# Kernel optimization log

Hardware: AMD Instinct MI355X
Metric: run time of the kernel (lower is better)

The kernel has to match this reference:

```python
import jax, jax.numpy as jnp
import numpy as np

B, NB, H, E, NCT, NL = 16, 4096, 128, 65536, 32, 2
LN_EPS = 1e-5


def _layernorm(x, scale, bias):
    mu = jnp.mean(x, axis=-1, keepdims=True)
    var = jnp.var(x, axis=-1, keepdims=True)
    return (x - mu) / jnp.sqrt(var + LN_EPS) * scale + bias


def setup_inputs() -> dict:
    key = jax.random.key(0)
    ks = jax.random.split(key, 18)
    s = 1.0 / np.sqrt(H)
    inp = {
        'block_tokens': jax.random.normal(ks[0], (B, NB, H), jnp.float32),
        'edge_structure': jnp.full((E,), 0.5, jnp.float32),
        'ct_emb': 0.1 * jax.random.normal(ks[1], (NCT, E), jnp.float32),
        'W_proj': s * jax.random.normal(ks[2], (H, H), jnp.float32),
        'b_proj': jnp.zeros((H,), jnp.float32),
        'W_gate': (1.0 / np.sqrt(2 * H)) * jax.random.normal(ks[3], (2 * H, H), jnp.float32),
        'b_gate': jnp.zeros((H,), jnp.float32),
        'ln_scale': jnp.ones((NL, H), jnp.float32),
        'ln_bias': jnp.zeros((NL, H), jnp.float32),
        'W1': s * jax.random.normal(ks[4], (NL, H, 2 * H), jnp.float32),
        'b1': jnp.zeros((NL, 2 * H), jnp.float32),
        'W2': (1.0 / np.sqrt(2 * H)) * jax.random.normal(ks[5], (NL, 2 * H, H), jnp.float32),
        'b2': jnp.zeros((NL, H), jnp.float32),
        'cancer_type': jax.random.randint(ks[6], (B,), 0, NCT),
        'edge_src': jax.random.randint(ks[7], (E,), 0, NB),
        'edge_dst': jax.random.randint(ks[8], (E,), 0, NB),
        'block_active': jax.random.bernoulli(ks[9], 0.9, (B, NB)),
    }
    return inp


def reference(block_tokens, edge_structure, ct_emb, W_proj, b_proj, W_gate, b_gate,
              ln_scale, ln_bias, W1, b1, W2, b2,
              cancer_type, edge_src, edge_dst, block_active):
    # per-edge signed weights, masked by active src/dst blocks  -> (B, E)
    structure = jax.nn.sigmoid(edge_structure)
    edge_w = structure[None, :] * ct_emb[cancer_type]
    edge_w = edge_w * block_active[:, edge_src].astype(edge_w.dtype) \
                    * block_active[:, edge_dst].astype(edge_w.dtype)
    # route projection + ELU
    h_route = jax.nn.elu(jnp.einsum('bnh,hd->bnd', block_tokens, W_proj) + b_proj)
    # gather sources, weight, scatter-add to destinations
    weighted = edge_w[..., None] * h_route[:, edge_src, :]          # (B, E, H)
    messages = jnp.zeros_like(block_tokens).at[:, edge_dst, :].add(weighted)
    # gated residual
    gate = jax.nn.sigmoid(
        jnp.einsum('bnh,hd->bnd', jnp.concatenate([block_tokens, messages], axis=-1), W_gate) + b_gate)
    x = block_tokens + gate * messages
    # norm + FFN layers (dropout is identity at inference)
    for l in range(NL):
        normed = _layernorm(x, ln_scale[l], ln_bias[l])
        h = jax.nn.elu(jnp.einsum('bnh,hf->bnf', normed, W1[l]) + b1[l])
        x = x + jnp.einsum('bnf,fh->bnh', h, W2[l]) + b2[l]
    return (x, edge_w)
```

## Files before the change

kernel.cpp:

```cpp
#include <hip/hip_runtime.h>
#include <hip/hip_bf16.h>

#define BB     16
#define NBLK   4096
#define HD     128
#define NE     65536
#define MTOT   (BB * NBLK)

typedef __attribute__((ext_vector_type(8))) short bf16x8;
typedef __attribute__((ext_vector_type(4))) float f32x4;

__device__ __forceinline__ float bf2f(unsigned short u) {
    union { unsigned int i; float f; } v; v.i = ((unsigned int)u) << 16; return v.f;
}
__device__ __forceinline__ unsigned short f2bf(float f) {
    union { float f; unsigned int i; } v; v.f = f;
    unsigned int u = v.i;
    unsigned int r = u + 0x7FFFu + ((u >> 16) & 1u);
    return (unsigned short)(r >> 16);
}
__device__ __forceinline__ float ldf(const void* p, size_t i, int f32m) {
    return f32m ? ((const float*)p)[i] : bf2f(((const unsigned short*)p)[i]);
}
__device__ __forceinline__ int get_active(const void* p, int i, int mode) {
    switch (mode) {
        case 1:  return ((const unsigned char*)p)[i] != 0;
        case 2:  return ((const unsigned short*)p)[i] != 0;
        case 3:  return ((const float*)p)[i] != 0.f;
        default: return ((const int*)p)[i] != 0;
    }
}

__global__ void probe_k(const unsigned int* __restrict__ es,
                        const unsigned int* __restrict__ act,
                        int* __restrict__ flags)
{
    const int lane = threadIdx.x;
    const unsigned int v0 = act[lane], v1 = act[64 + lane];
    auto le1  = [](unsigned int v) { return v <= 1u; };
    auto byt  = [](unsigned int v) {
        return ((v & 0xFFu) <= 1u) && (((v >> 8) & 0xFFu) <= 1u) &&
               (((v >> 16) & 0xFFu) <= 1u) && ((v >> 24) <= 1u); };
    auto f32b = [](unsigned int v) { return v == 0u || v == 0x3F800000u; };
    auto bfb  = [](unsigned int v) {
        unsigned short h0 = (unsigned short)(v & 0xFFFFu), h1 = (unsigned short)(v >> 16);
        return (h0 == 0u || h0 == 0x3F80u) && (h1 == 0u || h1 == 0x3F80u); };
    const unsigned long long m_le1 = __ballot(le1(v0) && le1(v1));
    const unsigned long long m_byt = __ballot(byt(v0) && byt(v1));
    const unsigned long long m_f32 = __ballot(f32b(v0) && f32b(v1));
    const unsigned long long m_bf  = __ballot(bfb(v0) && bfb(v1));
    if (lane == 0) {
        flags[0] = (es[0] != 0x3F003F00u) ? 1 : 0;
        const unsigned long long full = ~0ull;
        flags[1] = (m_le1 == full) ? 0
                 : (m_byt == full) ? 1
                 : (m_f32 == full) ? 3
                 : (m_bf  == full) ? 2 : 0;
    }
}

__global__ __launch_bounds__(256) void cvt_k(const void* __restrict__ bt,
                                             unsigned short* __restrict__ bt16,
                                             const int* __restrict__ flags)
{
    const size_t i = ((size_t)blockIdx.x * 256 + threadIdx.x) * 8;
    if (flags[0]) {
        const float* q = (const float*)bt + i;
        f32x4 lo = *(const f32x4*)q;
        f32x4 hi = *(const f32x4*)(q + 4);
        bf16x8 r;
        #pragma unroll
        for (int j = 0; j < 4; ++j) { r[j] = (short)f2bf(lo[j]); r[4 + j] = (short)f2bf(hi[j]); }
        *(bf16x8*)(bt16 + i) = r;
    } else {
        *(bf16x8*)(bt16 + i) = *(const bf16x8*)((const unsigned short*)bt + i);
    }
}

__global__ __launch_bounds__(256) void transpose_k(
    const void* p0, const void* p1, const void* p2, const void* p3,
    const void* p4, const void* p5, unsigned short* __restrict__ wsT,
    const int* __restrict__ flags)
{
    const void* srcs[6]  = {p0, p1, p2, p3, p4, p5};
    const int eoffs[6]   = {0, 0, 0, 32768, 0, 32768};
    const int Ks[6]      = {128, 256, 128, 128, 256, 256};
    const int nsh[6]     = {7,   7,   8,   8,   7,   7};
    const int offs[6]    = {0, 16384, 49152, 81920, 114688, 147456};
    const int f32m = flags[0];
    const int z = blockIdx.y;
    const int K = Ks[z];
    const int Nn = 1 << nsh[z];
    const int idx = blockIdx.x * 256 + threadIdx.x;
    if (idx >= K * Nn) return;
    const int k = idx >> nsh[z];
    const int n = idx & (Nn - 1);
    wsT[offs[z] + n * K + k] = f2bf(ldf(srcs[z], (size_t)eoffs[z] + idx, f32m));
}

__global__ __launch_bounds__(256) void csr_count_k(const int* __restrict__ edst,
                                                   int* __restrict__ cnt)
{
    const int e = blockIdx.x * 256 + threadIdx.x;
    atomicAdd(&cnt[edst[e]], 1);
}

__global__ __launch_bounds__(1024) void csr_scan_k(const int* __restrict__ cnt,
                                                   int* __restrict__ ofs,
                                                   int* __restrict__ cur)
{
    __shared__ int part[1024];
    const int t = threadIdx.x;
    const int4 c = ((const int4*)cnt)[t];
    part[t] = c.x + c.y + c.z + c.w;
    __syncthreads();
    #pragma unroll
    for (int off = 1; off < 1024; off <<= 1) {
        const int v = (t >= off) ? part[t - off] : 0;
        __syncthreads();
        part[t] += v;
        __syncthreads();
    }
    const int base = t ? part[t - 1] : 0;
    int4 o;
    o.x = base; o.y = o.x + c.x; o.z = o.y + c.y; o.w = o.z + c.z;
    ((int4*)ofs)[t] = o;
    ((int4*)cur)[t] = o;
    if (t == 1023) ofs[4096] = part[1023];
}

__global__ __launch_bounds__(256) void csr_fill_k(const int* __restrict__ edst,
                                                  int* __restrict__ cur,
                                                  int* __restrict__ eidx,
                                                  int* __restrict__ pos_e)
{
    const int e = blockIdx.x * 256 + threadIdx.x;
    const int pos = atomicAdd(&cur[edst[e]], 1);
    eidx[pos] = e;
    pos_e[e] = pos;
}

__global__ __launch_bounds__(256) void edge_k(
    const void* __restrict__ es, const void* __restrict__ ctE,
    const int* __restrict__ ctype, const int* __restrict__ esrc, const int* __restrict__ edst,
    const void* __restrict__ act, const int* __restrict__ pos_e,
    float* __restrict__ out_ew, float2* __restrict__ compact,
    const int* __restrict__ flags)
{
    const int f32m = flags[0], am = flags[1];
    const int idx = blockIdx.x * 256 + threadIdx.x;
    const int b = idx >> 16;
    const int e = idx & 65535;
    const int s = esrc[e];
    const float sv  = 1.f / (1.f + expf(-ldf(es, e, f32m)));
    const float emb = ldf(ctE, (size_t)ctype[b] * NE + e, f32m);
    const int a1 = get_active(act, b * NBLK + s, am);
    const int a2 = get_active(act, b * NBLK + edst[e], am);
    const float w = (a1 && a2) ? sv * emb : 0.f;
    out_ew[idx] = w;
    compact[((size_t)b << 16) + pos_e[e]] = make_float2(w, __int_as_float(s));
}

__global__ __launch_bounds__(256) void gather_k(
    const float2* __restrict__ compact, const int* __restrict__ ofs,
    const unsigned short* __restrict__ hr, unsigned short* __restrict__ msg)
{
    const int blk = blockIdx.x;
    const int xcd = blk & 7;
    const int i   = blk >> 3;
    const int b   = xcd * 2 + (i & 1);
    const int d   = ((i >> 1) << 2) | (threadIdx.x >> 6);
    const int lane = threadIdx.x & 63;
    const int sub  = lane >> 4;
    const int l15  = lane & 15;
    const int j1 = ofs[d + 1];
    const size_t bbase = (size_t)b * NBLK * HD;
    const float2* cb = compact + ((size_t)b << 16);
    float acc[8];
    #pragma unroll
    for (int i2 = 0; i2 < 8; ++i2) acc[i2] = 0.f;
    int j = ofs[d] + sub;
    float2 c = (j < j1) ? cb[j] : make_float2(0.f, 0.f);
    while (j < j1) {
        const int jn = j + 4;
        const float2 cn = (jn < j1) ? cb[jn] : make_float2(0.f, 0.f);
        if (c.x != 0.f) {
            const int src = __float_as_int(c.y);
            const bf16x8 v = *(const bf16x8*)(hr + bbase + (size_t)src * HD + l15 * 8);
            #pragma unroll
            for (int i2 = 0; i2 < 8; ++i2)
                acc[i2] += c.x * bf2f((unsigned short)v[i2]);
        }
        c = cn; j = jn;
    }
    #pragma unroll
    for (int i2 = 0; i2 < 8; ++i2) {
        acc[i2] += __shfl_xor(acc[i2], 16);
        acc[i2] += __shfl_xor(acc[i2], 32);
    }
    if (sub == 0) {
        bf16x8 o;
        #pragma unroll
        for (int i2 = 0; i2 < 8; ++i2) o[i2] = (short)f2bf(acc[i2]);
        *(bf16x8*)(msg + bbase + (size_t)d * HD + l15 * 8) = o;
    }
}

template<int K, int N, int EPI>
__global__ __launch_bounds__(256) void gemm_k(
    const unsigned short* __restrict__ A,
    const unsigned short* __restrict__ A2,
    const unsigned short* __restrict__ WT,
    const void* __restrict__ bias, long boff,
    const void* __restrict__ btf,
    float* __restrict__ outf,
    unsigned short* __restrict__ outb,
    const int* __restrict__ flags)
{
    constexpr int KI    = K / 32;
    constexpr int NCW   = N / 4;
    constexpr int NTW   = NCW / 16;
    constexpr int TILES = 4;
    constexpr int NBUF  = (K == 128 ? 4 : 2);
    const int f32m = flags[0];
    const int t    = threadIdx.x;
    const int lane = t & 63;
    const int wave = t >> 6;
    const int q    = lane >> 4;
    const int l15  = lane & 15;
    const int n0   = wave * NCW;

    bf16x8 Bf[KI][NTW];
    #pragma unroll
    for (int ki = 0; ki < KI; ++ki)
        #pragma unroll
        for (int nt = 0; nt < NTW; ++nt)
            Bf[ki][nt] = *(const bf16x8*)(WT + (size_t)(n0 + nt * 16 + l15) * K + ki * 32 + q * 8);

    float biasv[NTW];
    #pragma unroll
    for (int nt = 0; nt < NTW; ++nt)
        biasv[nt] = ldf(bias, boff + n0 + nt * 16 + l15, f32m);

    const int tile0 = blockIdx.x * TILES;
    bf16x8 Af[NBUF][KI];
    auto loadA = [&](int tt) {
        const int arow = (tile0 + tt) * 16 + l15;
        #pragma unroll
        for (int ki = 0; ki < KI; ++ki) {
            const int k = ki * 32 + q * 8;
            if constexpr (EPI == 1) {
                Af[tt % NBUF][ki] = (k < HD)
                    ? *(const bf16x8*)(A  + (size_t)arow * HD + k)
                    : *(const bf16x8*)(A2 + (size_t)arow * HD + (k - HD));
            } else {
                Af[tt % NBUF][ki] = *(const bf16x8*)(A + (size_t)arow * K + k);
            }
        }
    };
    #pragma unroll
    for (int p = 0; p < NBUF; ++p) loadA(p);

    #pragma unroll
    for (int tt = 0; tt < TILES; ++tt) {
        const int s = tt % NBUF;
        f32x4 acc[NTW];
        #pragma unroll
        for (int i = 0; i < NTW; ++i) acc[i] = (f32x4){0.f, 0.f, 0.f, 0.f};
        #pragma unroll
        for (int ki = 0; ki < KI; ++ki)
            #pragma unroll
            for (int nt = 0; nt < NTW; ++nt)
                acc[nt] = __builtin_amdgcn_mfma_f32_16x16x32_bf16(Af[s][ki], Bf[ki][nt], acc[nt], 0, 0, 0);

        if (tt + NBUF < TILES) loadA(tt + NBUF);

        const int m0 = (tile0 + tt) * 16;
        #pragma unroll
        for (int nt = 0; nt < NTW; ++nt) {
            #pragma unroll
            for (int r = 0; r < 4; ++r) {
                const int row = m0 + q * 4 + r;
                const int col = n0 + nt * 16 + l15;
                const size_t oidx = (size_t)row * N + col;
                float v = acc[nt][r] + biasv[nt];
                if constexpr (EPI == 0 || EPI == 2) {
                    outb[oidx] = f2bf(v > 0.f ? v : expm1f(v));
                } else if constexpr (EPI == 1) {
                    const float g = 1.f / (1.f + expf(-v));
                    outf[oidx] = ldf(btf, oidx, f32m) + g * bf2f(A2[oidx]);
                } else {
                    outf[oidx] += v;
                }
            }
        }
    }
}

__global__ __launch_bounds__(256) void fused_layer_k(
    float* __restrict__ x,
    const unsigned short* __restrict__ W1T,
    const unsigned short* __restrict__ W2T,
    const void* __restrict__ b1, long b1off,
    const void* __restrict__ b2, long b2off,
    const void* __restrict__ lns, long soff,
    const void* __restrict__ lnb, long loff,
    const int* __restrict__ flags)
{
    constexpr int R = 32;
    __shared__ __align__(16) float          x_lds[R][132];
    __shared__ __align__(16) unsigned short nrm_lds[R][136];
    __shared__ __align__(16) unsigned short h_lds[R][264];

    const int f32m = flags[0];
    const int t    = threadIdx.x;
    const int lane = t & 63;
    const int wave = t >> 6;
    const int q    = lane >> 4;
    const int l15  = lane & 15;

    const int row = t >> 3;
    const int seg = t & 7;
    const float* xp = x + ((size_t)blockIdx.x * R + row) * HD + seg * 16;
    f32x4 xv[4];
    #pragma unroll
    for (int j = 0; j < 4; ++j) xv[j] = *(const f32x4*)(xp + j * 4);

    const int n1 = wave * 64;
    bf16x8 B1[4][4];
    #pragma unroll
    for (int ki = 0; ki < 4; ++ki)
        #pragma unroll
        for (int nt = 0; nt < 4; ++nt)
            B1[ki][nt] = *(const bf16x8*)(W1T + (size_t)(n1 + nt * 16 + l15) * 128 + ki * 32 + q * 8);
    float bias1[4];
    #pragma unroll
    for (int nt = 0; nt < 4; ++nt) bias1[nt] = ldf(b1, b1off + n1 + nt * 16 + l15, f32m);

    float s = 0.f, ss = 0.f;
    #pragma unroll
    for (int j = 0; j < 4; ++j)
        #pragma unroll
        for (int k = 0; k < 4; ++k) { const float v = xv[j][k]; s += v; ss += v * v; }
    #pragma unroll
    for (int off = 1; off < 8; off <<= 1) { s += __shfl_xor(s, off); ss += __shfl_xor(ss, off); }
    const float mu = s * (1.f / 128.f);
    const float rs = rsqrtf(ss * (1.f / 128.f) - mu * mu + 1e-5f);

    #pragma unroll
    for (int j = 0; j < 4; ++j) *(f32x4*)&x_lds[row][seg * 16 + j * 4] = xv[j];
    bf16x8 nv[2];
    #pragma unroll
    for (int j = 0; j < 4; ++j)
        #pragma unroll
        for (int k = 0; k < 4; ++k) {
            const int col = seg * 16 + j * 4 + k;
            const float nn = (xv[j][k] - mu) * rs * ldf(lns, soff + col, f32m)
                             + ldf(lnb, loff + col, f32m);
            nv[j >> 1][(j & 1) * 4 + k] = (short)f2bf(nn);
        }
    *(bf16x8*)&nrm_lds[row][seg * 16]     = nv[0];
    *(bf16x8*)&nrm_lds[row][seg * 16 + 8] = nv[1];
    __syncthreads();

    #pragma unroll
    for (int tt = 0; tt < 2; ++tt) {
        bf16x8 Af[4];
        #pragma unroll
        for (int ki = 0; ki < 4; ++ki)
            Af[ki] = *(const bf16x8*)&nrm_lds[tt * 16 + l15][ki * 32 + q * 8];
        f32x4 acc[4];
        #pragma unroll
        for (int nt = 0; nt < 4; ++nt) acc[nt] = (f32x4){0.f, 0.f, 0.f, 0.f};
        #pragma unroll
        for (int ki = 0; ki < 4; ++ki)
            #pragma unroll
            for (int nt = 0; nt < 4; ++nt)
                acc[nt] = __builtin_amdgcn_mfma_f32_16x16x32_bf16(Af[ki], B1[ki][nt], acc[nt], 0, 0, 0);
        #pragma unroll
        for (int nt = 0; nt < 4; ++nt)
            #pragma unroll
            for (int r = 0; r < 4; ++r) {
                const float v = acc[nt][r] + bias1[nt];
                h_lds[tt * 16 + q * 4 + r][n1 + nt * 16 + l15] =
                    f2bf(v > 0.f ? v : expm1f(v));
            }
    }

    const int n2 = wave * 32;
    bf16x8 B2[8][2];
    #pragma unroll
    for (int ki = 0; ki < 8; ++ki)
        #pragma unroll
        for (int nt = 0; nt < 2; ++nt)
            B2[ki][nt] = *(const bf16x8*)(W2T + (size_t)(n2 + nt * 16 + l15) * 256 + ki * 32 + q * 8);
    float bias2[2];
    #pragma unroll
    for (int nt = 0; nt < 2; ++nt) bias2[nt] = ldf(b2, b2off + n2 + nt * 16 + l15, f32m);
    __syncthreads();

    #pragma unroll
    for (int tt = 0; tt < 2; ++tt) {
        bf16x8 Ah[8];
        #pragma unroll
        for (int ki = 0; ki < 8; ++ki)
            Ah[ki] = *(const bf16x8*)&h_lds[tt * 16 + l15][ki * 32 + q * 8];
        f32x4 acc[2];
        #pragma unroll
        for (int nt = 0; nt < 2; ++nt) acc[nt] = (f32x4){0.f, 0.f, 0.f, 0.f};
        #pragma unroll
        for (int ki = 0; ki < 8; ++ki)
            #pragma unroll
            for (int nt = 0; nt < 2; ++nt)
                acc[nt] = __builtin_amdgcn_mfma_f32_16x16x32_bf16(Ah[ki], B2[ki][nt], acc[nt], 0, 0, 0);
        #pragma unroll
        for (int nt = 0; nt < 2; ++nt)
            #pragma unroll
            for (int r = 0; r < 4; ++r)
                x_lds[tt * 16 + q * 4 + r][n2 + nt * 16 + l15] += acc[nt][r] + bias2[nt];
    }
    __syncthreads();

    float* xout = x + (size_t)blockIdx.x * R * HD;
    #pragma unroll
    for (int j = 0; j < 4; ++j) {
        const int idx = j * 256 + t;
        const int r2  = idx >> 5;
        const int c4  = (idx & 31) * 4;
        *(f32x4*)(xout + (size_t)idx * 4) = *(const f32x4*)&x_lds[r2][c4];
    }
}

extern "C" void kernel_launch(void* const* d_in, const int* in_sizes, int n_in,
                              void* d_out, int out_size, void* d_ws, size_t ws_size,
                              hipStream_t stream)
{
    (void)in_sizes; (void)n_in; (void)out_size; (void)ws_size;

    const void* bt  = d_in[0];
    const void* es  = d_in[1];
    const void* ctE = d_in[2];
    const void* Wp  = d_in[3];
    const void* bp  = d_in[4];
    const void* Wg  = d_in[5];
    const void* bg  = d_in[6];
    const void* lns = d_in[7];
    const void* lnb = d_in[8];
    const void* W1  = d_in[9];
    const void* b1  = d_in[10];
    const void* W2  = d_in[11];
    const void* b2  = d_in[12];
    const int* ctype = (const int*)d_in[13];
    const int* esrc  = (const int*)d_in[14];
    const int* edst  = (const int*)d_in[15];
    const void* act  = d_in[16];

    float* out_x  = (float*)d_out;
    float* out_ew = out_x + (size_t)MTOT * HD;
    float* x = out_x;

    char* ws = (char*)d_ws;
    int*            flags = (int*)ws;
    unsigned short* msg   = (unsigned short*)(ws + 1024);
    unsigned short* bt16  = (unsigned short*)(ws + 1024 + (16ull << 20));
    unsigned short* hr    = (unsigned short*)(ws + 1024 + (32ull << 20));
    char* base48 = ws + 1024 + (48ull << 20);
    int*            cnt     = (int*)(base48);
    int*            ofs     = (int*)(base48 + (16 << 10));
    int*            cur     = (int*)(base48 + (36 << 10));
    int*            eidx    = (int*)(base48 + (52 << 10));
    int*            pos_e   = (int*)(base48 + (308 << 10));
    unsigned short* WT      = (unsigned short*)(base48 + (576 << 10));
    float2*         compact = (float2*)(base48 + (1 << 20));

    const int M = MTOT;

    probe_k<<<1, 64, 0, stream>>>((const unsigned int*)es, (const unsigned int*)act, flags);
    hipMemsetAsync(cnt, 0, NBLK * sizeof(int), stream);

    cvt_k<<<dim3((M * HD / 8) / 256), 256, 0, stream>>>(bt, bt16, flags);
    transpose_k<<<dim3(128, 6), 256, 0, stream>>>(Wp, Wg, W1, W1, W2, W2, WT, flags);

    csr_count_k<<<dim3(NE / 256), 256, 0, stream>>>(edst, cnt);
    csr_scan_k<<<dim3(1), 1024, 0, stream>>>(cnt, ofs, cur);
    csr_fill_k<<<dim3(NE / 256), 256, 0, stream>>>(edst, cur, eidx, pos_e);

    edge_k<<<dim3((BB * NE) / 256), 256, 0, stream>>>(
        es, ctE, ctype, esrc, edst, act, pos_e, out_ew, compact, flags);

    gemm_k<128, 128, 0><<<dim3(M / 64), 256, 0, stream>>>(
        bt16, nullptr, WT + 0, bp, 0, nullptr, nullptr, hr, flags);

    gather_k<<<dim3(M / 4), 256, 0, stream>>>(compact, ofs, hr, msg);

    gemm_k<256, 128, 1><<<dim3(M / 64), 256, 0, stream>>>(
        bt16, msg, WT + 16384, bg, 0, bt, x, nullptr, flags);

    fused_layer_k<<<dim3(M / 32), 256, 0, stream>>>(
        x, WT + 49152, WT + 114688, b1, 0, b2, 0, lns, 0, lnb, 0, flags);
    fused_layer_k<<<dim3(M / 32), 256, 0, stream>>>(
        x, WT + 81920, WT + 147456, b1, 256, b2, 128, lns, 128, lnb, 128, flags);
}
```

Before: 347.9 us.

## Fuse gate GEMM and both FFN layers into one kernel keeping x in LDS

Replaces the separate gated-residual GEMM and the two per-layer fused FFN kernels with a single kernel. It computes the gate and residual for a 32-row tile into LDS, then runs both layernorm+FFN layers on that tile without writing x to global memory in between. This removes three launches and several full fp32 round trips of x (64K×128 floats). It also switches ELU and sigmoid to fast __expf, which costs a little accuracy near zero for ELU. The trade-off is higher register pressure from the gate weights plus per-layer weight reloads inside one block.

```diff
diff --git a/kernel.cpp b/kernel.cpp
--- a/kernel.cpp
+++ b/kernel.cpp
@@ -29,6 +29,13 @@
         case 3:  return ((const float*)p)[i] != 0.f;
         default: return ((const int*)p)[i] != 0;
     }
+}
+__device__ __forceinline__ float elu_f(float v) {
+    const float e = __expf(v);
+    return v > 0.f ? v : e - 1.f;
+}
+__device__ __forceinline__ float sig_f(float v) {
+    return 1.f / (1.f + __expf(-v));
 }
 
 __global__ void probe_k(const unsigned int* __restrict__ es,
@@ -152,7 +159,7 @@
     const int b = idx >> 16;
     const int e = idx & 65535;
     const int s = esrc[e];
-    const float sv  = 1.f / (1.f + expf(-ldf(es, e, f32m)));
+    const float sv  = sig_f(ldf(es, e, f32m));
     const float emb = ldf(ctE, (size_t)ctype[b] * NE + e, f32m);
     const int a1 = get_active(act, b * NBLK + s, am);
     const int a2 = get_active(act, b * NBLK + edst[e], am);
@@ -209,11 +216,8 @@
 template<int K, int N, int EPI>
 __global__ __launch_bounds__(256) void gemm_k(
     const unsigned short* __restrict__ A,
-    const unsigned short* __restrict__ A2,
     const unsigned short* __restrict__ WT,
     const void* __restrict__ bias, long boff,
-    const void* __restrict__ btf,
-    float* __restrict__ outf,
     unsigned short* __restrict__ outb,
     const int* __restrict__ flags)
 {
@@ -247,16 +251,8 @@
     auto loadA = [&](int tt) {
         const int arow = (tile0 + tt) * 16 + l15;
         #pragma unroll
-        for (int ki = 0; ki < KI; ++ki) {
-            const int k = ki * 32 + q * 8;
-            if constexpr (EPI == 1) {
-                Af[tt % NBUF][ki] = (k < HD)
-                    ? *(const bf16x8*)(A  + (size_t)arow * HD + k)
-                    : *(const bf16x8*)(A2 + (size_t)arow * HD + (k - HD));
-            } else {
-                Af[tt % NBUF][ki] = *(const bf16x8*)(A + (size_t)arow * K + k);
-            }
-        }
+        for (int ki = 0; ki < KI; ++ki)
+            Af[tt % NBUF][ki] = *(const bf16x8*)(A + (size_t)arow * K + ki * 32 + q * 8);
     };
     #pragma unroll
     for (int p = 0; p < NBUF; ++p) loadA(p);
@@ -282,29 +278,22 @@
             for (int r = 0; r < 4; ++r) {
                 const int row = m0 + q * 4 + r;
                 const int col = n0 + nt * 16 + l15;
-                const size_t oidx = (size_t)row * N + col;
-                float v = acc[nt][r] + biasv[nt];
-                if constexpr (EPI == 0 || EPI == 2) {
-                    outb[oidx] = f2bf(v > 0.f ? v : expm1f(v));
-                } else if constexpr (EPI == 1) {
-                    const float g = 1.f / (1.f + expf(-v));
-                    outf[oidx] = ldf(btf, oidx, f32m) + g * bf2f(A2[oidx]);
-                } else {
-                    outf[oidx] += v;
-                }
+                const float v = acc[nt][r] + biasv[nt];
+                outb[(size_t)row * N + col] = f2bf(elu_f(v));
             }
         }
     }
 }
 
-__global__ __launch_bounds__(256) void fused_layer_k(
-    float* __restrict__ x,
-    const unsigned short* __restrict__ W1T,
-    const unsigned short* __restrict__ W2T,
-    const void* __restrict__ b1, long b1off,
-    const void* __restrict__ b2, long b2off,
-    const void* __restrict__ lns, long soff,
-    const void* __restrict__ lnb, long loff,
+__global__ __launch_bounds__(256) void mega_k(
+    const unsigned short* __restrict__ bt16,
+    const unsigned short* __restrict__ msg,
+    const void* __restrict__ btf,
+    const unsigned short* __restrict__ WT,
+    const void* __restrict__ bg,
+    const void* __restrict__ b1, const void* __restrict__ b2,
+    const void* __restrict__ lns, const void* __restrict__ lnb,
+    float* __restrict__ xout,
     const int* __restrict__ flags)
 {
     constexpr int R = 32;
@@ -318,116 +307,177 @@
     const int wave = t >> 6;
     const int q    = lane >> 4;
     const int l15  = lane & 15;
-
-    const int row = t >> 3;
-    const int seg = t & 7;
-    const float* xp = x + ((size_t)blockIdx.x * R + row) * HD + seg * 16;
-    f32x4 xv[4];
-    #pragma unroll
-    for (int j = 0; j < 4; ++j) xv[j] = *(const f32x4*)(xp + j * 4);
-
+    const int row0 = blockIdx.x * R;
+
+    const int ng = wave * 32;
+    const unsigned short* WgT = WT + 16384;
+
+    bf16x8 Bg[8][2];
+    #pragma unroll
+    for (int ki = 0; ki < 8; ++ki)
+        #pragma unroll
+        for (int nt = 0; nt < 2; ++nt)
+            Bg[ki][nt] = *(const bf16x8*)(WgT + (size_t)(ng + nt * 16 + l15) * 256 + ki * 32 + q * 8);
+    float biasg[2];
+    #pragma unroll
+    for (int nt = 0; nt < 2; ++nt) biasg[nt] = ldf(bg, ng + nt * 16 + l15, f32m);
+
+    bf16x8 Ag[2][8];
+    #pragma unroll
+    for (int tt = 0; tt < 2; ++tt) {
+        const int arow = row0 + tt * 16 + l15;
+        #pragma unroll
+        for (int ki = 0; ki < 8; ++ki) {
+            const int k = ki * 32 + q * 8;
+            Ag[tt][ki] = (k < HD)
+                ? *(const bf16x8*)(bt16 + (size_t)arow * HD + k)
+                : *(const bf16x8*)(msg  + (size_t)arow * HD + (k - HD));
+        }
+    }
+
+    float btv[2][2][4], mgv[2][2][4];
+    #pragma unroll
+    for (int tt = 0; tt < 2; ++tt)
+        #pragma unroll
+        for (int nt = 0; nt < 2; ++nt)
+            #pragma unroll
+            for (int r = 0; r < 4; ++r) {
+                const size_t gi = (size_t)(row0 + tt * 16 + q * 4 + r) * HD + ng + nt * 16 + l15;
+                btv[tt][nt][r] = ldf(btf, gi, f32m);
+                mgv[tt][nt][r] = bf2f(msg[gi]);
+            }
+
+    #pragma unroll
+    for (int tt = 0; tt < 2; ++tt) {
+        f32x4 acc[2];
+        #pragma unroll
+        for (int nt = 0; nt < 2; ++nt) acc[nt] = (f32x4){0.f, 0.f, 0.f, 0.f};
+        #pragma unroll
+        for (int ki = 0; ki < 8; ++ki)
+            #pragma unroll
+            for (int nt = 0; nt < 2; ++nt)
+                acc[nt] = __builtin_amdgcn_mfma_f32_16x16x32_bf16(Ag[tt][ki], Bg[ki][nt], acc[nt], 0, 0, 0);
+        #pragma unroll
+        for (int nt = 0; nt < 2; ++nt)
+            #pragma unroll
+            for (int r = 0; r < 4; ++r) {
+                const float g = sig_f(acc[nt][r] + biasg[nt]);
+                x_lds[tt * 16 + q * 4 + r][ng + nt * 16 + l15] =
+                    btv[tt][nt][r] + g * mgv[tt][nt][r];
+            }
+    }
+    __syncthreads();
+
+    const int rowln = t >> 3;
+    const int seg   = t & 7;
     const int n1 = wave * 64;
-    bf16x8 B1[4][4];
-    #pragma unroll
-    for (int ki = 0; ki < 4; ++ki)
-        #pragma unroll
-        for (int nt = 0; nt < 4; ++nt)
-            B1[ki][nt] = *(const bf16x8*)(W1T + (size_t)(n1 + nt * 16 + l15) * 128 + ki * 32 + q * 8);
-    float bias1[4];
-    #pragma unroll
-    for (int nt = 0; nt < 4; ++nt) bias1[nt] = ldf(b1, b1off + n1 + nt * 16 + l15, f32m);
-
-    float s = 0.f, ss = 0.f;
-    #pragma unroll
-    for (int j = 0; j < 4; ++j)
-        #pragma unroll
-        for (int k = 0; k < 4; ++k) { const float v = xv[j][k]; s += v; ss += v * v; }
-    #pragma unroll
-    for (int off = 1; off < 8; off <<= 1) { s += __shfl_xor(s, off); ss += __shfl_xor(ss, off); }
-    const float mu = s * (1.f / 128.f);
-    const float rs = rsqrtf(ss * (1.f / 128.f) - mu * mu + 1e-5f);
-
-    #pragma unroll
-    for (int j = 0; j < 4; ++j) *(f32x4*)&x_lds[row][seg * 16 + j * 4] = xv[j];
-    bf16x8 nv[2];
-    #pragma unroll
-    for (int j = 0; j < 4; ++j)
-        #pragma unroll
-        for (int k = 0; k < 4; ++k) {
-            const int col = seg * 16 + j * 4 + k;
-            const float nn = (xv[j][k] - mu) * rs * ldf(lns, soff + col, f32m)
-                             + ldf(lnb, loff + col, f32m);
-            nv[j >> 1][(j & 1) * 4 + k] = (short)f2bf(nn);
+    const int n2 = wave * 32;
+
+    #pragma unroll
+    for (int l = 0; l < 2; ++l) {
+        const unsigned short* W1T = WT + (l ? 81920  : 49152);
+        const unsigned short* W2T = WT + (l ? 147456 : 114688);
+        const long b1o = l ? 256 : 0, b2o = l ? 128 : 0, lno = l ? 128 : 0;
+
+        bf16x8 B1[4][4];
+        #pragma unroll
+        for (int ki = 0; ki < 4; ++ki)
+            #pragma unroll
+            for (int nt = 0; nt < 4; ++nt)
+                B1[ki][nt] = *(const bf16x8*)(W1T + (size_t)(n1 + nt * 16 + l15) * 128 + ki * 32 + q * 8);
+        float bias1[4];
+        #pragma unroll
+        for (int nt = 0; nt < 4; ++nt) bias1[nt] = ldf(b1, b1o + n1 + nt * 16 + l15, f32m);
+
+        f32x4 xv[4];
+        #pragma unroll
+        for (int j = 0; j < 4; ++j) xv[j] = *(const f32x4*)&x_lds[rowln][seg * 16 + j * 4];
+        float s = 0.f, ss = 0.f;
+        #pragma unroll
+        for (int j = 0; j < 4; ++j)
+            #pragma unroll
+            for (int k = 0; k < 4; ++k) { const float v = xv[j][k]; s += v; ss += v * v; }
+        #pragma unroll
+        for (int off = 1; off < 8; off <<= 1) { s += __shfl_xor(s, off); ss += __shfl_xor(ss, off); }
+        const float mu = s * (1.f / 128.f);
+        const float rs = rsqrtf(ss * (1.f / 128.f) - mu * mu + 1e-5f);
+        bf16x8 nv[2];
+        #pragma unroll
+        for (int j = 0; j < 4; ++j)
+            #pragma unroll
+            for (int k = 0; k < 4; ++k) {
+                const int col = seg * 16 + j * 4 + k;
+                const float nn = (xv[j][k] - mu) * rs * ldf(lns, lno + col, f32m)
+                                 + ldf(lnb, lno + col, f32m);
+                nv[j >> 1][(j & 1) * 4 + k] = (short)f2bf(nn);
+            }
+        *(bf16x8*)&nrm_lds[rowln][seg * 16]     = nv[0];
+        *(bf16x8*)&nrm_lds[rowln][seg * 16 + 8] = nv[1];
+        __syncthreads();
+
+        #pragma unroll
+        for (int tt = 0; tt < 2; ++tt) {
+            bf16x8 Af[4];
+            #pragma unroll
+            for (int ki = 0; ki < 4; ++ki)
+                Af[ki] = *(const bf16x8*)&nrm_lds[tt * 16 + l15][ki * 32 + q * 8];
+            f32x4 acc[4];
+            #pragma unroll
+            for (int nt = 0; nt < 4; ++nt) acc[nt] = (f32x4){0.f, 0.f, 0.f, 0.f};
+            #pragma unroll
+            for (int ki = 0; ki < 4; ++ki)
+                #pragma unroll
+                for (int nt = 0; nt < 4; ++nt)
+                    acc[nt] = __builtin_amdgcn_mfma_f32_16x16x32_bf16(Af[ki], B1[ki][nt], acc[nt], 0, 0, 0);
+            #pragma unroll
+            for (int nt = 0; nt < 4; ++nt)
+                #pragma unroll
+                for (int r = 0; r < 4; ++r)
+                    h_lds[tt * 16 + q * 4 + r][n1 + nt * 16 + l15] =
+                        f2bf(elu_f(acc[nt][r] + bias1[nt]));
         }
-    *(bf16x8*)&nrm_lds[row][seg * 16]     = nv[0];
-    *(bf16x8*)&nrm_lds[row][seg * 16 + 8] = nv[1];
-    __syncthreads();
-
-    #pragma unroll
-    for (int tt = 0; tt < 2; ++tt) {
-        bf16x8 Af[4];
-        #pragma unroll
-        for (int ki = 0; ki < 4; ++ki)
-            Af[ki] = *(const bf16x8*)&nrm_lds[tt * 16 + l15][ki * 32 + q * 8];
-        f32x4 acc[4];
-        #pragma unroll
-        for (int nt = 0; nt < 4; ++nt) acc[nt] = (f32x4){0.f, 0.f, 0.f, 0.f};
-        #pragma unroll
-        for (int ki = 0; ki < 4; ++ki)
-            #pragma unroll
-            for (int nt = 0; nt < 4; ++nt)
-                acc[nt] = __builtin_amdgcn_mfma_f32_16x16x32_bf16(Af[ki], B1[ki][nt], acc[nt], 0, 0, 0);
-        #pragma unroll
-        for (int nt = 0; nt < 4; ++nt)
-            #pragma unroll
-            for (int r = 0; r < 4; ++r) {
-                const float v = acc[nt][r] + bias1[nt];
-                h_lds[tt * 16 + q * 4 + r][n1 + nt * 16 + l15] =
-                    f2bf(v > 0.f ? v : expm1f(v));
-            }
-    }
-
-    const int n2 = wave * 32;
-    bf16x8 B2[8][2];
-    #pragma unroll
-    for (int ki = 0; ki < 8; ++ki)
-        #pragma unroll
-        for (int nt = 0; nt < 2; ++nt)
-            B2[ki][nt] = *(const bf16x8*)(W2T + (size_t)(n2 + nt * 16 + l15) * 256 + ki * 32 + q * 8);
-    float bias2[2];
-    #pragma unroll
-    for (int nt = 0; nt < 2; ++nt) bias2[nt] = ldf(b2, b2off + n2 + nt * 16 + l15, f32m);
-    __syncthreads();
-
-    #pragma unroll
-    for (int tt = 0; tt < 2; ++tt) {
-        bf16x8 Ah[8];
+
+        bf16x8 B2[8][2];
         #pragma unroll
         for (int ki = 0; ki < 8; ++ki)
-            Ah[ki] = *(const bf16x8*)&h_lds[tt * 16 + l15][ki * 32 + q * 8];
-        f32x4 acc[2];
-        #pragma unroll
-        for (int nt = 0; nt < 2; ++nt) acc[nt] = (f32x4){0.f, 0.f, 0.f, 0.f};
-        #pragma unroll
-        for (int ki = 0; ki < 8; ++ki)
             #pragma unroll
             for (int nt = 0; nt < 2; ++nt)
-                acc[nt] = __builtin_amdgcn_mfma_f32_16x16x32_bf16(Ah[ki], B2[ki][nt], acc[nt], 0, 0, 0);
-        #pragma unroll
-        for (int nt = 0; nt < 2; ++nt)
-            #pragma unroll
-            for (int r = 0; r < 4; ++r)
-                x_lds[tt * 16 + q * 4 + r][n2 + nt * 16 + l15] += acc[nt][r] + bias2[nt];
-    }
-    __syncthreads();
-
-    float* xout = x + (size_t)blockIdx.x * R * HD;
+                B2[ki][nt] = *(const bf16x8*)(W2T + (size_t)(n2 + nt * 16 + l15) * 256 + ki * 32 + q * 8);
+        float bias2[2];
+        #pragma unroll
+        for (int nt = 0; nt < 2; ++nt) bias2[nt] = ldf(b2, b2o + n2 + nt * 16 + l15, f32m);
+        __syncthreads();
+
+        #pragma unroll
+        for (int tt = 0; tt < 2; ++tt) {
+            bf16x8 Ah[8];
+            #pragma unroll
+            for (int ki = 0; ki < 8; ++ki)
+                Ah[ki] = *(const bf16x8*)&h_lds[tt * 16 + l15][ki * 32 + q * 8];
+            f32x4 acc[2];
+            #pragma unroll
+            for (int nt = 0; nt < 2; ++nt) acc[nt] = (f32x4){0.f, 0.f, 0.f, 0.f};
+            #pragma unroll
+            for (int ki = 0; ki < 8; ++ki)
+                #pragma unroll
+                for (int nt = 0; nt < 2; ++nt)
+                    acc[nt] = __builtin_amdgcn_mfma_f32_16x16x32_bf16(Ah[ki], B2[ki][nt], acc[nt], 0, 0, 0);
+            #pragma unroll
+            for (int nt = 0; nt < 2; ++nt)
+                #pragma unroll
+                for (int r = 0; r < 4; ++r)
+                    x_lds[tt * 16 + q * 4 + r][n2 + nt * 16 + l15] += acc[nt][r] + bias2[nt];
+        }
+        __syncthreads();
+    }
+
+    float* xo = xout + (size_t)row0 * HD;
     #pragma unroll
     for (int j = 0; j < 4; ++j) {
         const int idx = j * 256 + t;
         const int r2  = idx >> 5;
         const int c4  = (idx & 31) * 4;
-        *(f32x4*)(xout + (size_t)idx * 4) = *(const f32x4*)&x_lds[r2][c4];
+        *(f32x4*)(xo + (size_t)idx * 4) = *(const f32x4*)&x_lds[r2][c4];
     }
 }
 
@@ -489,15 +539,10 @@
         es, ctE, ctype, esrc, edst, act, pos_e, out_ew, compact, flags);
 
     gemm_k<128, 128, 0><<<dim3(M / 64), 256, 0, stream>>>(
-        bt16, nullptr, WT + 0, bp, 0, nullptr, nullptr, hr, flags);
+        bt16, WT + 0, bp, 0, hr, flags);
 
     gather_k<<<dim3(M / 4), 256, 0, stream>>>(compact, ofs, hr, msg);
 
-    gemm_k<256, 128, 1><<<dim3(M / 64), 256, 0, stream>>>(
-        bt16, msg, WT + 16384, bg, 0, bt, x, nullptr, flags);
-
-    fused_layer_k<<<dim3(M / 32), 256, 0, stream>>>(
-        x, WT + 49152, WT + 114688, b1, 0, b2, 0, lns, 0, lnb, 0, flags);
-    fused_layer_k<<<dim3(M / 32), 256, 0, stream>>>(
-        x, WT + 81920, WT + 147456, b1, 256, b2, 128, lns, 128, lnb, 128, flags);
-}
+    mega_k<<<dim3(M / 32), 256, 0, stream>>>(
+        bt16, msg, bt, WT, bg, b1, b2, lns, lnb, x, flags);
+}
```

Measured after the change: 327.7 us. 1.06x faster.
